# Kernel tuning notes

Hardware: AMD Instinct MI355X
Metric: run time of the kernel (lower is better)

Reference implementation:

```python
import jax, jax.numpy as jnp
import numpy as np

N_DRUGS = 4096; N_GENE = 5414; N_KG = N_DRUGS + N_GENE
N_MOL = 131072; E_MOL = 524288; E_KG = 524288; R = 8
MLP_IN = 1024; MLP_H = 512; D = 256; GCN_IN = 64; GCN_H = 128
DIM1 = 256; DIM2 = 128; DIM3 = 64; NCLS = 2
EPS = 1e-5


def setup_inputs() -> dict:
    key = jax.random.key(0)
    ks = jax.random.split(key, 32)
    def n(i, shape, fan):
        return jax.random.normal(ks[i], shape, dtype=jnp.float32) * (1.0 / np.sqrt(fan))
    inp = {}
    inp['fp_data'] = jax.random.normal(ks[0], (N_DRUGS, MLP_IN), dtype=jnp.float32)
    inp['mol_x'] = jax.random.normal(ks[1], (N_MOL, GCN_IN), dtype=jnp.float32)
    inp['mol_batch'] = jnp.sort(jax.random.randint(ks[2], (N_MOL,), 0, N_DRUGS))
    inp['mol_edge_index'] = jax.random.randint(ks[3], (2, E_MOL), 0, N_MOL)
    inp['kg_edge_index'] = jax.random.randint(ks[4], (2, E_KG), 0, N_KG)
    inp['kg_edge_type'] = jax.random.randint(ks[5], (E_KG,), 0, R)
    # parameters
    inp['fp_w1'] = n(6, (MLP_IN, MLP_H), MLP_IN); inp['fp_b1'] = jnp.zeros((MLP_H,), jnp.float32)
    inp['fp_w2'] = n(7, (MLP_H, D), MLP_H);       inp['fp_b2'] = jnp.zeros((D,), jnp.float32)
    inp['gcn_w1'] = n(8, (GCN_IN, GCN_H), GCN_IN); inp['gcn_b1'] = jnp.zeros((GCN_H,), jnp.float32)
    inp['gcn_w2'] = n(9, (GCN_H, D), GCN_H);       inp['gcn_b2'] = jnp.zeros((D,), jnp.float32)
    inp['att_w1'] = n(10, (D, 128), D); inp['att_b1'] = jnp.zeros((128,), jnp.float32)
    inp['att_w2'] = n(11, (128,), 128)
    inp['gene_emb'] = jax.random.normal(ks[12], (N_GENE, D), dtype=jnp.float32)
    inp['rg_w1'] = n(13, (R, D, DIM1), D); inp['rg_root1'] = n(14, (D, DIM1), D); inp['rg_b1'] = jnp.zeros((DIM1,), jnp.float32)
    inp['rg_w2'] = n(15, (R, DIM1, DIM2), DIM1); inp['rg_root2'] = n(16, (DIM1, DIM2), DIM1); inp['rg_b2'] = jnp.zeros((DIM2,), jnp.float32)
    inp['lin1_w'] = n(17, (DIM2, DIM3), DIM2); inp['lin1_b'] = jnp.zeros((DIM3,), jnp.float32)
    inp['lin2_w'] = n(18, (DIM3, NCLS), DIM3); inp['lin2_b'] = jnp.zeros((NCLS,), jnp.float32)
    return inp


def bn(x):
    # BatchNorm1d with batch statistics (gamma=1, beta=0)
    m = jnp.mean(x, axis=0, keepdims=True)
    v = jnp.var(x, axis=0, keepdims=True)
    return (x - m) * jax.lax.rsqrt(v + EPS)


def gcn_conv(x, w, b, src, dst, num_nodes):
    # PyG GCNConv: self-loops + symmetric normalization
    loop = jnp.arange(num_nodes, dtype=src.dtype)
    src = jnp.concatenate([src, loop]); dst = jnp.concatenate([dst, loop])
    h = x @ w  # [N, F]
    deg = jnp.zeros((num_nodes,), x.dtype).at[dst].add(1.0)
    dinv = jax.lax.rsqrt(jnp.maximum(deg, 1.0))
    norm = dinv[src] * dinv[dst]  # [E]
    out = jnp.zeros_like(h).at[dst].add(h[src] * norm[:, None])
    return out + b


def rgcn_conv(x, w, root, b, src, dst, etype, num_nodes):
    # PyG RGCNConv (aggr='mean' per relation): out_i = x_i @ root + b + sum_r mean_{j in N_r(i)} x_j @ W_r
    h = jnp.einsum('nd,rdf->rnf', x, w)          # [R, N, F]
    msg = h[etype, src]                          # [E, F] gather by (relation, source)
    cnt = jnp.zeros((R, num_nodes), x.dtype).at[etype, dst].add(1.0)
    norm = 1.0 / jnp.maximum(cnt[etype, dst], 1.0)  # [E]
    agg = jnp.zeros((num_nodes, w.shape[-1]), x.dtype).at[dst].add(msg * norm[:, None])
    return agg + x @ root + b


def forward(fp_data, mol_x, mol_batch, mol_edge_index, kg_edge_index, kg_edge_type,
            fp_w1, fp_b1, fp_w2, fp_b2, gcn_w1, gcn_b1, gcn_w2, gcn_b2,
            att_w1, att_b1, att_w2, gene_emb,
            rg_w1, rg_root1, rg_b1, rg_w2, rg_root2, rg_b2,
            lin1_w, lin1_b, lin2_w, lin2_b):
    # fingerprint MLP branch
    fp = jax.nn.relu(bn(fp_data @ fp_w1 + fp_b1))
    fp = jax.nn.relu(bn(fp @ fp_w2 + fp_b2))      # [N_DRUGS, D]
    # molecular GCN branch (batched graph replaces the dataloader loop)
    msrc, mdst = mol_edge_index[0], mol_edge_index[1]
    g = jax.nn.relu(bn(gcn_conv(mol_x, gcn_w1, gcn_b1, msrc, mdst, N_MOL)))
    g = jax.nn.relu(bn(gcn_conv(g, gcn_w2, gcn_b2, msrc, mdst, N_MOL)))  # [N_MOL, D]
    # global mean pool per molecule
    gsum = jnp.zeros((N_DRUGS, D), g.dtype).at[mol_batch].add(g)
    gcnt = jnp.zeros((N_DRUGS,), g.dtype).at[mol_batch].add(1.0)
    graph_out = gsum / jnp.maximum(gcnt, 1.0)[:, None]  # [N_DRUGS, D]
    # attention fusion of the two views
    z = jnp.stack([graph_out, fp], axis=1)        # [N_DRUGS, 2, D]
    w = jnp.tanh(z @ att_w1 + att_b1) @ att_w2    # [N_DRUGS, 2]
    beta = jax.nn.softmax(w, axis=1)
    emb = jnp.sum(beta[:, :, None] * z, axis=1)   # [N_DRUGS, D]
    # knowledge graph RGCN over drugs + genes
    x = jnp.concatenate([emb, gene_emb], axis=0)  # [N_KG, D]
    ksrc, kdst = kg_edge_index[0], kg_edge_index[1]
    x = jax.nn.relu(bn(rgcn_conv(x, rg_w1, rg_root1, rg_b1, ksrc, kdst, kg_edge_type, N_KG)))
    x = jax.nn.relu(bn(rgcn_conv(x, rg_w2, rg_root2, rg_b2, ksrc, kdst, kg_edge_type, N_KG)))
    x = jax.nn.relu(bn(x @ lin1_w + lin1_b))
    x = x @ lin2_w + lin2_b
    return jax.nn.log_softmax(x, axis=-1), beta[:, :, None]


def reference(fp_data, mol_x, mol_batch, mol_edge_index, kg_edge_index, kg_edge_type,
              fp_w1, fp_b1, fp_w2, fp_b2, gcn_w1, gcn_b1, gcn_w2, gcn_b2,
              att_w1, att_b1, att_w2, gene_emb,
              rg_w1, rg_root1, rg_b1, rg_w2, rg_root2, rg_b2,
              lin1_w, lin1_b, lin2_w, lin2_b):
    return forward(fp_data, mol_x, mol_batch, mol_edge_index, kg_edge_index, kg_edge_type,
                   fp_w1, fp_b1, fp_w2, fp_b2, gcn_w1, gcn_b1, gcn_w2, gcn_b2,
                   att_w1, att_b1, att_w2, gene_emb,
                   rg_w1, rg_root1, rg_b1, rg_w2, rg_root2, rg_b2,
                   lin1_w, lin1_b, lin2_w, lin2_b)
```

## Files before the change

kernel.cpp:

```cpp
#include <hip/hip_runtime.h>
#include <hip/hip_bf16.h>
#include <cstdint>

typedef __hip_bfloat16 bf16;
typedef unsigned short u16;
typedef unsigned int u32;
typedef __attribute__((ext_vector_type(8))) short short8;
typedef __attribute__((ext_vector_type(4))) float f32x4;

__device__ __forceinline__ float tofloat(float x){ return x; }
__device__ __forceinline__ float tofloat(bf16 x){ return __bfloat162float(x); }
__device__ __forceinline__ float b2f(u16 a){ return __uint_as_float(((unsigned)a) << 16); }
__device__ __forceinline__ u16 f2b(float f){
    unsigned u = __float_as_uint(f);
    return (u16)((u + 0x7FFFu + ((u >> 16) & 1u)) >> 16);
}

static inline int divup(long a, long b){ return (int)((a + b - 1) / b); }

#define NBLK_STATS 256

__global__ void zero_int(int* p){ *p = 0; }

__global__ void detect_f32(const u16* __restrict__ h, long n, int* flag)
{
    long i = (long)blockIdx.x * blockDim.x + threadIdx.x;
    long st = (long)gridDim.x * blockDim.x;
    int c = 0;
    for (; i < n; i += st)
        if (((h[i] >> 7) & 0xFF) == 0xFF) c++;
    if (c) atomicAdd(flag, c);
}

struct ConvTab { const void* src[14]; float* dst[14]; u16* dstB[14]; int n[14]; };

__global__ void conv_all(ConvTab t, const int* __restrict__ flagp)
{
    bool f32 = (*flagp != 0);
    int seg = blockIdx.y;
    const void* s = t.src[seg];
    float* d = t.dst[seg];
    u16*   dB = t.dstB[seg];
    int n = t.n[seg];
    long i = (long)blockIdx.x * blockDim.x + threadIdx.x;
    long st = (long)gridDim.x * blockDim.x;
    for (; i < n; i += st) {
        float v = f32 ? ((const float*)s)[i] : tofloat(((const bf16*)s)[i]);
        d[i] = v; dB[i] = f2b(v);
    }
}

__global__ void conv_in(const void* __restrict__ src, float* __restrict__ dst,
                        long n, const int* __restrict__ flagp)
{
    bool f32 = (*flagp != 0);
    long i = (long)blockIdx.x * blockDim.x + threadIdx.x;
    long st = (long)gridDim.x * blockDim.x;
    for (; i < n; i += st)
        dst[i] = f32 ? ((const float*)src)[i] : tofloat(((const bf16*)src)[i]);
}

__global__ void conv_dual_b16(const void* __restrict__ src, u16* __restrict__ dst,
                              long n, const int* __restrict__ flagp)
{
    bool f32 = (*flagp != 0);
    long i = (long)blockIdx.x * blockDim.x + threadIdx.x;
    long st = (long)gridDim.x * blockDim.x;
    for (; i < n; i += st)
        dst[i] = f32 ? f2b(((const float*)src)[i]) : ((const u16*)src)[i];
}

__global__ void conv_f32_b16(const float* __restrict__ src, u16* __restrict__ dst, long n)
{
    long i = (long)blockIdx.x * blockDim.x + threadIdx.x;
    long st = (long)gridDim.x * blockDim.x;
    for (; i < n; i += st) dst[i] = f2b(src[i]);
}

__global__ void conv_molx(const float* __restrict__ src, u16* __restrict__ dst,
                          long n4, const int* __restrict__ flagp)
{
    if (*flagp == 0) return;
    long i = (long)blockIdx.x * blockDim.x + threadIdx.x;
    long st = (long)gridDim.x * blockDim.x;
    for (; i < n4; i += st) {
        float4 v = ((const float4*)src)[i];
        ushort4 o;
        o.x = f2b(v.x); o.y = f2b(v.y); o.z = f2b(v.z); o.w = f2b(v.w);
        ((ushort4*)dst)[i] = o;
    }
}

__global__ __launch_bounds__(256)
void transpose_b16(const u16* __restrict__ src, u16* __restrict__ dst, int K, int N)
{
    __shared__ u16 t[32][33];
    int k0 = blockIdx.x * 32, n0 = blockIdx.y * 32;
    int x = threadIdx.x & 31, y = threadIdx.x >> 5;
    for (int yy = y; yy < 32; yy += 8) {
        int k = k0 + yy, n = n0 + x;
        t[yy][x] = (k < K && n < N) ? src[(long)k * N + n] : (u16)0;
    }
    __syncthreads();
    for (int yy = y; yy < 32; yy += 8) {
        int n = n0 + yy, k = k0 + x;
        if (n < N && k < K) dst[(long)n * K + k] = t[x][yy];
    }
}

__global__ void flatten_mol(const int* __restrict__ bins, const int* __restrict__ src,
                            const float* __restrict__ en, long E, int2* __restrict__ out)
{
    long i = (long)blockIdx.x * blockDim.x + threadIdx.x;
    long st = (long)gridDim.x * blockDim.x;
    for (; i < E; i += st) {
        int e = bins[i];
        out[i] = make_int2(src[e], __float_as_int(en[e]));
    }
}

__global__ void kg_key2(const int* __restrict__ dst, const int* __restrict__ et,
                        long E, int* __restrict__ key)
{
    long i = (long)blockIdx.x * blockDim.x + threadIdx.x;
    long st = (long)gridDim.x * blockDim.x;
    for (; i < E; i += st) key[i] = dst[i] * 8 + et[i];
}

__global__ void flatten_kg_src(const int* __restrict__ bins, const int* __restrict__ src,
                               long E, int* __restrict__ out)
{
    long i = (long)blockIdx.x * blockDim.x + threadIdx.x;
    long st = (long)gridDim.x * blockDim.x;
    for (; i < E; i += st) out[i] = src[bins[i]];
}

template<typename TC, int NBLK, bool STATS>
__global__ __launch_bounds__(256)
void gemm_bt(const u16* __restrict__ A, int lda,
             const u16* __restrict__ BT, int ldbt,
             TC* __restrict__ C, int ldc,
             int M, int N, int K,
             float* __restrict__ SP1, float* __restrict__ SP2, int Ntot)
{
    __shared__ __align__(16) u16 As[64][40];
    __shared__ __align__(16) u16 Bs[NBLK * 64][40];
    __shared__ float st1[NBLK * 64], st2[NBLK * 64];
    const int tid = threadIdx.x;
    const int lane = tid & 63, wave = tid >> 6;
    const int l15 = lane & 15, quad = lane >> 4;
    const int wm = (wave & 1) * 32, wn = (wave >> 1) * 32;
    const int row0 = blockIdx.x * 64, col0 = blockIdx.y * (NBLK * 64);
    const int arow = tid >> 2, ak = (tid & 3) * 8;
    const int aok = row0 + arow < M;

    if (STATS && tid < NBLK * 64) { st1[tid] = 0.f; st2[tid] = 0.f; }

    f32x4 acc[NBLK][2][2];
#pragma unroll
    for (int t = 0; t < NBLK; t++)
#pragma unroll
        for (int i = 0; i < 2; i++)
#pragma unroll
            for (int j = 0; j < 2; j++)
#pragma unroll
                for (int r = 0; r < 4; r++) acc[t][i][j][r] = 0.f;

    const u16* pa = A + (long)(row0 + arow) * lda + ak;
    const u16* pb[NBLK];
#pragma unroll
    for (int t = 0; t < NBLK; t++)
        pb[t] = BT + (long)(col0 + t * 64 + arow) * ldbt + ak;

    ushort4 ra0 = {0,0,0,0}, ra1 = {0,0,0,0};
    ushort4 rb0[NBLK], rb1[NBLK];
    if (aok) { ra0 = *(const ushort4*)pa; ra1 = *(const ushort4*)(pa + 4); }
#pragma unroll
    for (int t = 0; t < NBLK; t++) {
        rb0[t] = *(const ushort4*)pb[t];
        rb1[t] = *(const ushort4*)(pb[t] + 4);
    }

    for (int k0 = 0; k0 < K; k0 += 32) {
        *(ushort4*)&As[arow][ak]     = ra0;
        *(ushort4*)&As[arow][ak + 4] = ra1;
#pragma unroll
        for (int t = 0; t < NBLK; t++) {
// ... 69 lines not shown

__global__ __launch_bounds__(256)
void gemm64(const float* __restrict__ A, int lda,
            const float* __restrict__ B, int ldb,
            float* __restrict__ C, int ldc,
            int M, int N, int K)
{
    __shared__ float As[16][68];
    __shared__ float Bs[16][68];
    const int tid = threadIdx.x;
    const int row0 = blockIdx.x * 64, col0 = blockIdx.y * 64;
    float acc[4][4];
#pragma unroll
    for (int i = 0; i < 4; i++)
#pragma unroll
        for (int j = 0; j < 4; j++) acc[i][j] = 0.f;
    const int ar = tid >> 2, ak = (tid & 3) * 4;
    const int bk = tid >> 4, bc = (tid & 15) * 4;
    const int ty4 = (tid >> 4) * 4, tx4 = (tid & 15) * 4;
    for (int k0 = 0; k0 < K; k0 += 16) {
        {
            int row = row0 + ar;
            float4 v = make_float4(0.f, 0.f, 0.f, 0.f);
            if (row < M) v = *(const float4*)(A + (long)row * lda + k0 + ak);
            As[ak + 0][ar] = v.x; As[ak + 1][ar] = v.y;
            As[ak + 2][ar] = v.z; As[ak + 3][ar] = v.w;
        }
        {
            int c = col0 + bc;
            float4 v = make_float4(0.f, 0.f, 0.f, 0.f);
            if (c < N) v = *(const float4*)(B + (long)(k0 + bk) * ldb + c);
            *(float4*)&Bs[bk][bc] = v;
        }
        __syncthreads();
#pragma unroll
        for (int k = 0; k < 16; k++) {
            float4 a = *(const float4*)&As[k][ty4];
            float4 b = *(const float4*)&Bs[k][tx4];
            acc[0][0] += a.x * b.x; acc[0][1] += a.x * b.y; acc[0][2] += a.x * b.z; acc[0][3] += a.x * b.w;
            acc[1][0] += a.y * b.x; acc[1][1] += a.y * b.y; acc[1][2] += a.y * b.z; acc[1][3] += a.y * b.w;
            acc[2][0] += a.z * b.x; acc[2][1] += a.z * b.y; acc[2][2] += a.z * b.z; acc[2][3] += a.z * b.w;
            acc[3][0] += a.w * b.x; acc[3][1] += a.w * b.y; acc[3][2] += a.w * b.z; acc[3][3] += a.w * b.w;
        }
        __syncthreads();
    }
    int c = col0 + tx4;
#pragma unroll
    for (int i = 0; i < 4; i++) {
        int r = row0 + ty4 + i;
        if (r < M && c < N)
            *(float4*)&C[(long)r * ldc + c] =
                make_float4(acc[i][0], acc[i][1], acc[i][2], acc[i][3]);
    }
}

__global__ void filli(int* p, long n, int v)
{
    long i = (long)blockIdx.x * blockDim.x + threadIdx.x;
    long st = (long)gridDim.x * blockDim.x;
    for (; i < n; i += st) p[i] = v;
}

__global__ void hist_int(const int* __restrict__ key, long n, int* __restrict__ h)
{
    long i = (long)blockIdx.x * blockDim.x + threadIdx.x;
    long st = (long)gridDim.x * blockDim.x;
    for (; i < n; i += st) atomicAdd(&h[key[i]], 1);
}

__global__ __launch_bounds__(1024)
void scan_bsum(const int* __restrict__ in, int n, int* __restrict__ btot)
{
    __shared__ int sh[1024];
    int tid = threadIdx.x;
    int i0 = blockIdx.x * 4096 + tid * 4;
    int s = 0;
#pragma unroll
    for (int t = 0; t < 4; t++) { int idx = i0 + t; s += (idx < n) ? in[idx] : 0; }
    sh[tid] = s;
    __syncthreads();
    for (int off = 512; off > 0; off >>= 1) {
        if (tid < off) sh[tid] += sh[tid + off];
        __syncthreads();
    }
    if (tid == 0) btot[blockIdx.x] = sh[0];
}

__global__ void scan_tiny(const int* __restrict__ btot, int nb, int* __restrict__ boff)
{
    if (threadIdx.x == 0) {
        int c = 0;
        for (int b = 0; b < nb; b++) { boff[b] = c; c += btot[b]; }
        boff[nb] = c;
    }
}

__global__ __launch_bounds__(1024)
void scan_final(const int* __restrict__ in, int n, const int* __restrict__ boff,
                int nb, int* __restrict__ out)
{
    __shared__ int buf[1024];
    int tid = threadIdx.x;
    int i0 = blockIdx.x * 4096 + tid * 4;
    int v[4]; int s = 0;
#pragma unroll
    for (int t = 0; t < 4; t++) {
        int idx = i0 + t;
        v[t] = (idx < n) ? in[idx] : 0;
        s += v[t];
    }
    buf[tid] = s;
    __syncthreads();
    for (int off = 1; off < 1024; off <<= 1) {
        int t = (tid >= off) ? buf[tid - off] : 0;
        __syncthreads();
        buf[tid] += t;
        __syncthreads();
    }
    int excl = buf[tid] - s + boff[blockIdx.x];
#pragma unroll
    for (int t = 0; t < 4; t++) {
        int idx = i0 + t;
        if (idx < n) out[idx] = excl;
        excl += v[t];
    }
    if (blockIdx.x == 0 && tid == 0) out[n] = boff[nb];
}

__global__ void bin_by(const int* __restrict__ key, long n,
                       const int* __restrict__ off, int* __restrict__ cursor,
                       int* __restrict__ bins)
{
    long i = (long)blockIdx.x * blockDim.x + threadIdx.x;
    long st = (long)gridDim.x * blockDim.x;
    for (; i < n; i += st) {
        int k = key[i];
        int pos = off[k] + atomicAdd(&cursor[k], 1);
        bins[pos] = (int)i;
    }
}

__global__ void dinv_from_deg(const int* __restrict__ deg, float* __restrict__ dinv, long n)
{
    long i = (long)blockIdx.x * blockDim.x + threadIdx.x;
    long st = (long)gridDim.x * blockDim.x;
    for (; i < n; i += st) dinv[i] = rsqrtf((float)(deg[i] + 1));
}

__global__ void mol_enorm(const int* __restrict__ src, const int* __restrict__ dst,
                          const float* __restrict__ dinv, long E, float* __restrict__ en)
{
    long i = (long)blockIdx.x * blockDim.x + threadIdx.x;
    long st = (long)gridDim.x * blockDim.x;
    for (; i < E; i += st) en[i] = dinv[src[i]] * dinv[dst[i]];
}

__global__ __launch_bounds__(256)
void colstats_f32_v2(const float* __restrict__ X, int M, int N,
                     float* __restrict__ p1, float* __restrict__ p2)
{
    __shared__ float sh1[1024], sh2[1024];
    int tid = threadIdx.x;
    int ncg = N >> 2;
    int cg  = tid & (ncg - 1);
    int rg  = tid / ncg;
    int nrg = 256 / ncg;
    float s0=0,s1=0,s2=0,s3=0, q0=0,q1=0,q2=0,q3=0;
    const float* base = X + 4 * cg;
    for (long row = (long)blockIdx.x * nrg + rg; row < M; row += (long)gridDim.x * nrg) {
        float4 v = *(const float4*)(base + row * (long)N);
        s0 += v.x; q0 += v.x * v.x; s1 += v.y; q1 += v.y * v.y;
        s2 += v.z; q2 += v.z * v.z; s3 += v.w; q3 += v.w * v.w;
    }
    float4* S1 = (float4*)sh1; float4* S2 = (float4*)sh2;
    S1[tid] = make_float4(s0, s1, s2, s3);
    S2[tid] = make_float4(q0, q1, q2, q3);
    __syncthreads();
    for (int off = nrg >> 1; off > 0; off >>= 1) {
        if (rg < off) {
            float4 a = S1[tid], b = S1[tid + off * ncg];
            S1[tid] = make_float4(a.x + b.x, a.y + b.y, a.z + b.z, a.w + b.w);
            float4 c = S2[tid], d = S2[tid + off * ncg];
            S2[tid] = make_float4(c.x + d.x, c.y + d.y, c.z + d.z, c.w + d.w);
        }
        __syncthreads();
    }
    if (rg == 0) {
        *(float4*)&p1[(long)blockIdx.x * N + 4 * cg] = S1[tid];
        *(float4*)&p2[(long)blockIdx.x * N + 4 * cg] = S2[tid];
    }
}

__global__ __launch_bounds__(1024)
void colstats_reduce_v3(const float* __restrict__ p1, const float* __restrict__ p2,
                        int nblk, int N, float invM,
                        float* __restrict__ s1o, float* __restrict__ s2o)
{
    __shared__ float sh1[1024], sh2[1024];
    int tid = threadIdx.x;
    int col = blockIdx.x * 64 + (tid & 63);
    int seg = tid >> 6;
    float a = 0.f, c = 0.f;
    for (int b = seg; b < nblk; b += 16) {
        a += p1[(long)b * N + col];
        c += p2[(long)b * N + col];
    }
    sh1[tid] = a; sh2[tid] = c;
// ... 63 lines not shown
    for (; j < j1; j++) {
        int2 e = eb[j];
        acc += b2f(X[(long)e.x * 64 + lane]) * __int_as_float(e.y);
    }
    out[(long)wid * 64 + lane] = f2b(acc);
}

__global__ __launch_bounds__(256)
void mol_agg128_bn(const u16* __restrict__ G, const float* __restrict__ dinv,
                   const int* __restrict__ off, const int2* __restrict__ eb,
                   int NM, const float* __restrict__ s1, const float* __restrict__ s2,
                   u16* __restrict__ out)
{
    int wid  = (int)(((long)blockIdx.x * 256 + threadIdx.x) >> 6);
    int lane = threadIdx.x & 63;
    if (wid >= NM) return;
    const float m0 = s1[2 * lane],     r0 = s2[2 * lane];
    const float m1 = s1[2 * lane + 1], r1 = s2[2 * lane + 1];
    float dv = dinv[wid], dv2 = dv * dv;
    u32 u = *(const u32*)(G + (long)wid * 128 + 2 * lane);
    float a0 = fmaxf((b2f((u16)(u & 0xFFFF)) - m0) * r0, 0.f) * dv2;
    float a1 = fmaxf((b2f((u16)(u >> 16))    - m1) * r1, 0.f) * dv2;
    int j = off[wid], j1 = off[wid + 1];
    for (; j + 3 < j1; j += 4) {
        int2 e0 = eb[j], e1 = eb[j + 1], e2 = eb[j + 2], e3 = eb[j + 3];
        u32 v0 = *(const u32*)(G + (long)e0.x * 128 + 2 * lane);
        u32 v1 = *(const u32*)(G + (long)e1.x * 128 + 2 * lane);
        u32 v2 = *(const u32*)(G + (long)e2.x * 128 + 2 * lane);
        u32 v3 = *(const u32*)(G + (long)e3.x * 128 + 2 * lane);
        float n0 = __int_as_float(e0.y), n1 = __int_as_float(e1.y);
        float n2 = __int_as_float(e2.y), n3 = __int_as_float(e3.y);
        a0 += fmaxf((b2f((u16)(v0 & 0xFFFF)) - m0) * r0, 0.f) * n0
            + fmaxf((b2f((u16)(v1 & 0xFFFF)) - m0) * r0, 0.f) * n1
            + fmaxf((b2f((u16)(v2 & 0xFFFF)) - m0) * r0, 0.f) * n2
            + fmaxf((b2f((u16)(v3 & 0xFFFF)) - m0) * r0, 0.f) * n3;
        a1 += fmaxf((b2f((u16)(v0 >> 16)) - m1) * r1, 0.f) * n0
            + fmaxf((b2f((u16)(v1 >> 16)) - m1) * r1, 0.f) * n1
            + fmaxf((b2f((u16)(v2 >> 16)) - m1) * r1, 0.f) * n2
            + fmaxf((b2f((u16)(v3 >> 16)) - m1) * r1, 0.f) * n3;
    }
    for (; j < j1; j++) {
        int2 e = eb[j];
        u32 v = *(const u32*)(G + (long)e.x * 128 + 2 * lane);
        float n = __int_as_float(e.y);
        a0 += fmaxf((b2f((u16)(v & 0xFFFF)) - m0) * r0, 0.f) * n;
        a1 += fmaxf((b2f((u16)(v >> 16))    - m1) * r1, 0.f) * n;
    }
    u32 o = (u32)f2b(a0) | ((u32)f2b(a1) << 16);
    *(u32*)(out + (long)wid * 128 + 2 * lane) = o;
}

__global__ __launch_bounds__(256)
void kg_preagg2(const u16* __restrict__ xin, const int* __restrict__ off2,
                const int* __restrict__ eb, int NSEG, u16* __restrict__ aggx)
{
    int seg  = (int)(((long)blockIdx.x * 256 + threadIdx.x) >> 6);
    int lane = threadIdx.x & 63;
    if (seg >= NSEG) return;
    int node = seg >> 3, r = seg & 7;
    const int c4 = 4 * lane;
    int j0 = off2[seg], j1 = off2[seg + 1];
    float a0 = 0.f, a1 = 0.f, a2 = 0.f, a3 = 0.f;
    int j = j0;
    for (; j + 3 < j1; j += 4) {
        int s0 = eb[j], s1 = eb[j + 1], s2 = eb[j + 2], s3 = eb[j + 3];
        ushort4 v0 = *(const ushort4*)(xin + (long)s0 * 256 + c4);
        ushort4 v1 = *(const ushort4*)(xin + (long)s1 * 256 + c4);
        ushort4 v2 = *(const ushort4*)(xin + (long)s2 * 256 + c4);
        ushort4 v3 = *(const ushort4*)(xin + (long)s3 * 256 + c4);
        a0 += b2f(v0.x) + b2f(v1.x) + b2f(v2.x) + b2f(v3.x);
        a1 += b2f(v0.y) + b2f(v1.y) + b2f(v2.y) + b2f(v3.y);
        a2 += b2f(v0.z) + b2f(v1.z) + b2f(v2.z) + b2f(v3.z);
        a3 += b2f(v0.w) + b2f(v1.w) + b2f(v2.w) + b2f(v3.w);
    }
    for (; j < j1; j++) {
        ushort4 v = *(const ushort4*)(xin + (long)eb[j] * 256 + c4);
        a0 += b2f(v.x); a1 += b2f(v.y); a2 += b2f(v.z); a3 += b2f(v.w);
    }
    float nrm = 1.0f / fmaxf((float)(j1 - j0), 1.0f);
    ushort4 o;
    o.x = f2b(a0 * nrm); o.y = f2b(a1 * nrm);
    o.z = f2b(a2 * nrm); o.w = f2b(a3 * nrm);
    *(ushort4*)(aggx + (long)node * 2304 + 256 + (r << 8) + c4) = o;
}

__global__ void xcopy_aggx(const u16* __restrict__ xin, u16* __restrict__ aggx, long n4)
{
    long i = (long)blockIdx.x * blockDim.x + threadIdx.x;
    long st = (long)gridDim.x * blockDim.x;
    for (; i < n4; i += st) {
        long node = i >> 6;
        int c4 = (int)(i & 63) * 4;
        *(ushort4*)(aggx + node * 2304 + c4) = *(const ushort4*)(xin + node * 256 + c4);
    }
}

__global__ __launch_bounds__(256)
void pool128(const u16* __restrict__ g, const int* __restrict__ off,
             const int* __restrict__ bins, int ND,
             const float* __restrict__ s1, const float* __restrict__ s2,
             float* __restrict__ gout, int c0out)
{
    int wid  = (int)(((long)blockIdx.x * 256 + threadIdx.x) >> 6);
    int lane = threadIdx.x & 63;
    if (wid >= ND) return;
    const float m0 = s1[2 * lane],     r0 = s2[2 * lane];
    const float m1 = s1[2 * lane + 1], r1 = s2[2 * lane + 1];
    int j0 = off[wid], j1 = off[wid + 1];
    float a0 = 0.f, a1 = 0.f;
    for (int j = j0; j < j1; j++) {
        u32 v = *(const u32*)(g + (long)bins[j] * 128 + 2 * lane);
        a0 += fmaxf((b2f((u16)(v & 0xFFFF)) - m0) * r0, 0.f);
        a1 += fmaxf((b2f((u16)(v >> 16))    - m1) * r1, 0.f);
    }
    float inv = 1.0f / fmaxf((float)(j1 - j0), 1.0f);
    *(float2*)(gout + (long)wid * 256 + c0out + 2 * lane) =
        make_float2(a0 * inv, a1 * inv);
}

__global__ void attention_fuse(const float* __restrict__ go, const float* __restrict__ fpv,
                               const float* __restrict__ fs1, const float* __restrict__ fs2,
                               const float* __restrict__ W1, const float* __restrict__ B1,
                               const float* __restrict__ W2,
                               float* __restrict__ emb, float* __restrict__ beta_out)
{
    int d = blockIdx.x;
    int t = threadIdx.x;
    __shared__ float z[2][256];
    __shared__ float red[128];
    for (int c = t; c < 256; c += 128) {
        z[0][c] = go[(long)d * 256 + c];
        z[1][c] = fmaxf((fpv[(long)d * 256 + c] - fs1[c]) * fs2[c], 0.f);
    }
    __syncthreads();
    float s[2];
    for (int v = 0; v < 2; v++) {
        float acc = B1[t];
        for (int k = 0; k < 256; k++) acc += z[v][k] * W1[k * 128 + t];
        red[t] = tanhf(acc) * W2[t];
        __syncthreads();
        for (int off = 64; off > 0; off >>= 1) {
            if (t < off) red[t] += red[t + off];
            __syncthreads();
        }
        s[v] = red[0];
        __syncthreads();
    }
    float m = fmaxf(s[0], s[1]);
    float e0 = expf(s[0] - m), e1 = expf(s[1] - m);
    float inv = 1.0f / (e0 + e1);
    float b0 = e0 * inv, b1 = e1 * inv;
    for (int c = t; c < 256; c += 128)
        emb[(long)d * 256 + c] = b0 * z[0][c] + b1 * z[1][c];
    if (t == 0) {
        beta_out[d * 2 + 0] = b0;
        beta_out[d * 2 + 1] = b1;
    }
}

__global__ void logits_out_bn(const float* __restrict__ x4,
                              const float* __restrict__ s1, const float* __restrict__ s2,
                              const float* __restrict__ w, const float* __restrict__ b,
                              float* __restrict__ out, int NKG)
{
    int i = blockIdx.x * blockDim.x + threadIdx.x;
    if (i >= NKG) return;
    float a0 = b[0], a1 = b[1];
    for (int k = 0; k < 64; k++) {
        float v = fmaxf((x4[(long)i * 64 + k] - s1[k]) * s2[k], 0.f);
        a0 += v * w[k * 2 + 0];
        a1 += v * w[k * 2 + 1];
    }
    float m = fmaxf(a0, a1);
    float lse = m + logf(expf(a0 - m) + expf(a1 - m));
    out[i * 2 + 0] = a0 - lse;
    out[i * 2 + 1] = a1 - lse;
}

extern "C" void kernel_launch(void* const* d_in, const int* in_sizes, int n_in,
                              void* d_out, int out_size, void* d_ws, size_t ws_size,
                              hipStream_t stream)
{
    (void)in_sizes; (void)n_in; (void)out_size; (void)ws_size;
    const int ND = 4096, NM = 131072, NKG = 9510, NGENE = 5414;
    const long EM = 524288, EK = 524288;
    const int NSEG = 8 * NKG;

    const void* fp_data = d_in[0];
    const void* mol_x   = d_in[1];
    const int*  mol_batch = (const int*)d_in[2];
    const int*  mol_ei  = (const int*)d_in[3];
    const int*  kg_ei   = (const int*)d_in[4];
    const int*  kg_et   = (const int*)d_in[5];

    const int* mol_src = mol_ei;
    const int* mol_dst = mol_ei + EM;
    const int* kg_src  = kg_ei;
    const int* kg_dst  = kg_ei + EK;

    float* out_ls   = (float*)d_out;
    float* out_beta = (float*)d_out + 19020;

    char* wp = (char*)d_ws;
    auto carve = [&](size_t bytes) { char* p = wp; wp += (bytes + 255) & ~(size_t)255; return p; };
    float* stats   = (float*)carve(4096);
    float* statsFP = (float*)carve(4096);
    int*   flag  = (int*)carve(256);
    float* dinv  = (float*)carve((size_t)NM * 4);
    float* enM   = (float*)carve((size_t)EM * 4);
    float* part1 = (float*)carve((size_t)2048 * 128 * 4);
    float* part2 = (float*)carve((size_t)2048 * 128 * 4);
    int*   sbt   = (int*)carve(256);
    int*   sbo   = (int*)carve(256);
    float* Wpool = (float*)carve((size_t)1630000 * 4);
    u16*   WpoolB= (u16*)carve((size_t)1630000 * 2);
    u16*   WpoolT= (u16*)carve((size_t)1600000 * 2);
    float* fpb   = (float*)carve((size_t)ND * 256 * 4);
    float* gout  = (float*)carve((size_t)ND * 256 * 4);
    int*   key2  = (int*)carve((size_t)EK * 4);
    int*   koff2 = (int*)carve((size_t)(NSEG + 1) * 4);
    char*  z0    = wp;
    int* kdeg2 = (int*)carve((size_t)NSEG * 4);
    int* kcur2 = (int*)carve((size_t)NSEG * 4);
    int* mdeg = (int*)carve((size_t)NM * 4);
    int* mcur = (int*)carve((size_t)NM * 4);
    int* pdeg = (int*)carve((size_t)ND * 4);
    int* pcur = (int*)carve((size_t)ND * 4);
    char*  z1    = wp;
    int* moff = (int*)carve((size_t)(NM + 1) * 4);
    int* mbins= (int*)carve((size_t)EM * 4);
    int* kbins= (int*)carve((size_t)EK * 4);
    int* poff = (int*)carve((size_t)(ND + 1) * 4);
    int* pbins= (int*)carve((size_t)NM * 4);
    char*  REG1  = carve((size_t)NM * 128 * 2);
    char*  REG2  = carve((size_t)NM * 128 * 2);
    u16*   HB    = (u16*)carve((size_t)NM * 64 * 2);

    u16*   XB  = (u16*)REG1;
    u16*   G1  = (u16*)REG1;
    u16*   H2  = (u16*)REG1;
    float* xkg = (float*)REG1;
    u16*   x2b = (u16*)REG1;
    float* x3  = (float*)REG1 + (size_t)NKG * 512;
    float* x4  = x3 + (size_t)NKG * 128;
    u16*   xb  = (u16*)(x4 + (size_t)NKG * 64);
    u16*   Xfb = (u16*)REG2;
    u16*   G1A = (u16*)REG2;
    u16*   AGGX= (u16*)REG2;
    u16*   fp1b = HB;
    u16*   Xagg = HB;
    int2* ebM  = (int2*)gout;
    int*  ebK2 = key2;

    zero_int<<<1, 1, 0, stream>>>(flag);
    detect_f32<<<1024, 256, 0, stream>>>((const u16*)fp_data, (long)ND * 1024, flag);
    ConvTab tab;
    const int widx[14] = {6, 8, 10, 12, 14, 15, 16, 19, 18, 22, 21, 24, 26, 27};
    const int wn[14]   = {1024*512, 512*256, 64*128, 128*256, 256*128, 128, 128,
                          256*256, 8*256*256, 256*128, 8*256*128, 128*64, 64*2, 2};
    float* wf[14]; u16* wb[14];
    {
        size_t o = 0;
        for (int i = 0; i < 14; i++) {
            tab.src[i]  = d_in[widx[i]];
            tab.dst[i]  = Wpool + o;
            tab.dstB[i] = WpoolB + o;
            tab.n[i]    = wn[i];
            wf[i] = Wpool + o; wb[i] = WpoolB + o;
            o += (size_t)wn[i];
        }
    }
    conv_all<<<dim3(32, 14), 256, 0, stream>>>(tab, flag);
    float *att_w1c = wf[4], *att_b1c = wf[5], *att_w2c = wf[6];
    float *lin1_wc = wf[11], *lin2_wc = wf[12], *lin2_bc = wf[13];

    u16* T_fpw1  = WpoolT;
    u16* T_fpw2  = T_fpw1 + (size_t)512 * 1024;
    u16* T_gcnw1 = T_fpw2 + (size_t)256 * 512;
    u16* T_gcnw2 = T_gcnw1 + (size_t)128 * 64;
    u16* T_w1    = T_gcnw2 + (size_t)256 * 128;
    u16* T_w2    = T_w1 + (size_t)256 * 2304;
    transpose_b16<<<dim3(32, 16), 256, 0, stream>>>(wb[0], T_fpw1, 1024, 512);
    transpose_b16<<<dim3(16, 8),  256, 0, stream>>>(wb[1], T_fpw2, 512, 256);
    transpose_b16<<<dim3(2, 4),   256, 0, stream>>>(wb[2], T_gcnw1, 64, 128);
    transpose_b16<<<dim3(4, 8),   256, 0, stream>>>(wb[3], T_gcnw2, 128, 256);
    transpose_b16<<<dim3(72, 8),  256, 0, stream>>>(wb[7], T_w1, 2304, 256);
    transpose_b16<<<dim3(72, 4),  256, 0, stream>>>(wb[9], T_w2, 2304, 128);

    filli<<<512, 256, 0, stream>>>((int*)z0, (long)(z1 - z0) / 4, 0);
    auto scan = [&](const int* deg, int* off, int n) {
        int nb = divup(n, 4096);
        scan_bsum<<<nb, 1024, 0, stream>>>(deg, n, sbt);
        scan_tiny<<<1, 64, 0, stream>>>(sbt, nb, sbo);
        scan_final<<<nb, 1024, 0, stream>>>(deg, n, sbo, nb, off);
    };
    hist_int<<<2048, 256, 0, stream>>>(mol_dst, EM, mdeg);
    scan(mdeg, moff, NM);
    bin_by<<<2048, 256, 0, stream>>>(mol_dst, EM, moff, mcur, mbins);
    dinv_from_deg<<<512, 256, 0, stream>>>(mdeg, dinv, NM);
    mol_enorm<<<1024, 256, 0, stream>>>(mol_src, mol_dst, dinv, EM, enM);
    flatten_mol<<<2048, 256, 0, stream>>>(mbins, mol_src, enM, EM, ebM);

    kg_key2<<<2048, 256, 0, stream>>>(kg_dst, kg_et, EK, key2);
    hist_int<<<2048, 256, 0, stream>>>(key2, EK, kdeg2);
    scan(kdeg2, koff2, NSEG);
    bin_by<<<2048, 256, 0, stream>>>(key2, EK, koff2, kcur2, kbins);
    flatten_kg_src<<<2048, 256, 0, stream>>>(kbins, kg_src, EK, ebK2);

    hist_int<<<512, 256, 0, stream>>>(mol_batch, NM, pdeg);
    scan(pdeg, poff, ND);
    bin_by<<<512, 256, 0, stream>>>(mol_batch, NM, poff, pcur, pbins);

    auto reduceNto = [&](int nblk, int N, float invM, float* s1o, float* s2o) {
        colstats_reduce_v3<<<N / 64, 1024, 0, stream>>>(part1, part2, nblk, N,
                                                        invM, s1o, s2o);
    };

    conv_dual_b16<<<2048, 256, 0, stream>>>(fp_data, Xfb, (long)ND * 1024, flag);
    gemm_bt<u16, 2, true><<<dim3(64, 4), 256, 0, stream>>>(
        Xfb, 1024, T_fpw1, 1024, fp1b, 512, ND, 512, 1024, part1, part2, 512);
    reduceNto(64, 512, 1.0f / ND, stats, stats + 512);
    bn_apply_b16v<<<2048, 256, 0, stream>>>((u32*)fp1b, (long)ND * 256, 255,
                                            stats, stats + 512);
    gemm_bt<float, 1, true><<<dim3(64, 4), 256, 0, stream>>>(
        fp1b, 512, T_fpw2, 512, fpb, 256, ND, 256, 512, part1, part2, 256);
    reduceNto(64, 256, 1.0f / ND, statsFP, statsFP + 512);

    conv_molx<<<2048, 256, 0, stream>>>((const float*)mol_x, XB, (long)NM * 16, flag);
    mol_agg_in<<<32768, 256, 0, stream>>>(mol_x, XB, flag, dinv, moff, ebM, NM, Xagg);
    gemm_bt<u16, 2, true><<<dim3(2048, 1), 256, 0, stream>>>(
        Xagg, 64, T_gcnw1, 64, G1, 128, NM, 128, 64, part1, part2, 128);
    reduceNto(2048, 128, 1.0f / NM, stats, stats + 512);

    mol_agg128_bn<<<32768, 256, 0, stream>>>(G1, dinv, moff, ebM, NM,
                                             stats, stats + 512, G1A);
    for (int h = 0; h < 2; h++) {
        gemm_bt<u16, 2, true><<<dim3(2048, 1), 256, 0, stream>>>(
            G1A, 128, T_gcnw2 + (size_t)h * 128 * 128, 128, H2, 128, NM, 128, 128,
            part1, part2, 128);
        reduceNto(2048, 128, 1.0f / NM, stats, stats + 512);
        pool128<<<1024, 256, 0, stream>>>(H2, poff, pbins, ND,
                                          stats, stats + 512, gout, h * 128);
    }

    attention_fuse<<<ND, 128, 0, stream>>>(gout, fpb, statsFP, statsFP + 512,
                                           att_w1c, att_b1c, att_w2c,
                                           xkg, out_beta);
    conv_in<<<512, 256, 0, stream>>>(d_in[17], xkg + (long)ND * 256,
                                     (long)NGENE * 256, flag);
    conv_f32_b16<<<1024, 256, 0, stream>>>(xkg, xb, (long)NKG * 256);

    xcopy_aggx<<<1024, 256, 0, stream>>>(xb, AGGX, (long)NKG * 64);
    kg_preagg2<<<divup((long)NSEG * 64, 256), 256, 0, stream>>>(
        xb, koff2, ebK2, NSEG, AGGX);
    gemm_bt<u16, 2, true><<<dim3(divup(NKG, 64), 2), 256, 0, stream>>>(
        AGGX, 2304, T_w1, 2304, x2b, 256, NKG, 256, 2304, part1, part2, 256);
    reduceNto(divup(NKG, 64), 256, 1.0f / NKG, stats, stats + 512);
    bn_apply_b16v<<<1024, 256, 0, stream>>>((u32*)x2b, (long)NKG * 128, 127,
                                            stats, stats + 512);

    xcopy_aggx<<<1024, 256, 0, stream>>>(x2b, AGGX, (long)NKG * 64);
    kg_preagg2<<<divup((long)NSEG * 64, 256), 256, 0, stream>>>(
        x2b, koff2, ebK2, NSEG, AGGX);
    gemm_bt<float, 1, true><<<dim3(divup(NKG, 64), 2), 256, 0, stream>>>(
        AGGX, 2304, T_w2, 2304, x3, 128, NKG, 128, 2304, part1, part2, 128);
    reduceNto(divup(NKG, 64), 128, 1.0f / NKG, stats, stats + 512);
    bn_apply<<<2048, 256, 0, stream>>>(x3, (long)NKG * 128, 127, stats, stats + 512);

    gemm64<<<dim3(divup(NKG, 64), 1, 1), 256, 0, stream>>>(
        x3, 128, lin1_wc, 64, x4, 64, NKG, 64, 128);
    colstats_f32_v2<<<NBLK_STATS, 256, 0, stream>>>(x4, NKG, 64, part1, part2);
    reduceNto(NBLK_STATS, 64, 1.0f / NKG, stats, stats + 512);
    logits_out_bn<<<divup(NKG, 256), 256, 0, stream>>>(x4, stats, stats + 512,
                                                       lin2_wc, lin2_bc, out_ls, NKG);
}
```

Measured before the change: 1.028 ms.

## Batch preprocessing kernels across graphs and fuse copy/convert launches

Merges the six weight transposes into one launch, and the three histogram, scan and bin passes (mol edges, KG edges, pooling batch) into multi-segment launches indexed by blockIdx. Edge-norm computation is folded into the mol flatten, and both flattens share one launch. Attention now writes bf16 directly and gene embeddings are converted straight to bf16, dropping the fp32 staging buffer. The self-feature copy into the aggregation buffer moves into kg_preagg2. The aim is fewer kernel launches and less memory traffic, at the cost of some idle blocks in the padded grids.

```diff
diff --git a/kernel.cpp b/kernel.cpp
--- a/kernel.cpp
+++ b/kernel.cpp
@@ -50,16 +50,6 @@
     }
 }
 
-__global__ void conv_in(const void* __restrict__ src, float* __restrict__ dst,
-                        long n, const int* __restrict__ flagp)
-{
-    bool f32 = (*flagp != 0);
-    long i = (long)blockIdx.x * blockDim.x + threadIdx.x;
-    long st = (long)gridDim.x * blockDim.x;
-    for (; i < n; i += st)
-        dst[i] = f32 ? ((const float*)src)[i] : tofloat(((const bf16*)src)[i]);
-}
-
 __global__ void conv_dual_b16(const void* __restrict__ src, u16* __restrict__ dst,
                               long n, const int* __restrict__ flagp)
 {
@@ -68,13 +58,6 @@
     long st = (long)gridDim.x * blockDim.x;
     for (; i < n; i += st)
         dst[i] = f32 ? f2b(((const float*)src)[i]) : ((const u16*)src)[i];
-}
-
-__global__ void conv_f32_b16(const float* __restrict__ src, u16* __restrict__ dst, long n)
-{
-    long i = (long)blockIdx.x * blockDim.x + threadIdx.x;
-    long st = (long)gridDim.x * blockDim.x;
-    for (; i < n; i += st) dst[i] = f2b(src[i]);
 }
 
 __global__ void conv_molx(const float* __restrict__ src, u16* __restrict__ dst,
@@ -91,31 +74,126 @@
     }
 }
 
+struct TransTab { const u16* src[6]; u16* dst[6]; int K[6]; int N[6]; };
+
 __global__ __launch_bounds__(256)
-void transpose_b16(const u16* __restrict__ src, u16* __restrict__ dst, int K, int N)
-{
-    __shared__ u16 t[32][33];
+void transpose6(TransTab t)
+{
+    int s = blockIdx.z;
+    int K = t.K[s], N = t.N[s];
     int k0 = blockIdx.x * 32, n0 = blockIdx.y * 32;
+    if (k0 >= K || n0 >= N) return;
+    const u16* src = t.src[s];
+    u16* dst = t.dst[s];
+    __shared__ u16 tl[32][33];
     int x = threadIdx.x & 31, y = threadIdx.x >> 5;
     for (int yy = y; yy < 32; yy += 8) {
         int k = k0 + yy, n = n0 + x;
-        t[yy][x] = (k < K && n < N) ? src[(long)k * N + n] : (u16)0;
+        tl[yy][x] = (k < K && n < N) ? src[(long)k * N + n] : (u16)0;
     }
     __syncthreads();
     for (int yy = y; yy < 32; yy += 8) {
         int n = n0 + yy, k = k0 + x;
-        if (n < N && k < K) dst[(long)n * K + k] = t[x][yy];
-    }
-}
-
-__global__ void flatten_mol(const int* __restrict__ bins, const int* __restrict__ src,
-                            const float* __restrict__ en, long E, int2* __restrict__ out)
-{
-    long i = (long)blockIdx.x * blockDim.x + threadIdx.x;
-    long st = (long)gridDim.x * blockDim.x;
-    for (; i < E; i += st) {
-        int e = bins[i];
-        out[i] = make_int2(src[e], __float_as_int(en[e]));
+        if (n < N && k < K) dst[(long)n * K + k] = tl[x][yy];
+    }
+}
+
+struct KV3 { const int* key[3]; int* h[3]; long n[3]; };
+
+__global__ void hist3(KV3 t)
+{
+    int s = blockIdx.y;
+    const int* key = t.key[s]; int* h = t.h[s]; long n = t.n[s];
+    long i = (long)blockIdx.x * blockDim.x + threadIdx.x;
+    long st = (long)gridDim.x * blockDim.x;
+    for (; i < n; i += st) atomicAdd(&h[key[i]], 1);
+}
+
+struct Scan3 { const int* in[3]; int* out[3]; int* bt[3]; int* bo[3]; int n[3]; };
+
+__global__ __launch_bounds__(1024)
+void scan_bsum3(Scan3 t)
+{
+    int s = blockIdx.y;
+    int n = t.n[s];
+    int nb = (n + 4095) >> 12;
+    if ((int)blockIdx.x >= nb) return;
+    const int* in = t.in[s];
+    __shared__ int sh[1024];
+    int tid = threadIdx.x;
+    int i0 = blockIdx.x * 4096 + tid * 4;
+    int acc = 0;
+#pragma unroll
+    for (int k = 0; k < 4; k++) { int idx = i0 + k; acc += (idx < n) ? in[idx] : 0; }
+    sh[tid] = acc;
+    __syncthreads();
+    for (int off = 512; off > 0; off >>= 1) {
+        if (tid < off) sh[tid] += sh[tid + off];
+        __syncthreads();
+    }
+    if (tid == 0) t.bt[s][blockIdx.x] = sh[0];
+}
+
+__global__ void scan_tiny3(Scan3 t)
+{
+    int s = blockIdx.x;
+    if (threadIdx.x != 0) return;
+    int nb = (t.n[s] + 4095) >> 12;
+    const int* bt = t.bt[s]; int* bo = t.bo[s];
+    int c = 0;
+    for (int b = 0; b < nb; b++) { bo[b] = c; c += bt[b]; }
+    bo[nb] = c;
+}
+
+__global__ __launch_bounds__(1024)
+void scan_final3(Scan3 t)
+{
+    int s = blockIdx.y;
+    int n = t.n[s];
+    int nb = (n + 4095) >> 12;
+    if ((int)blockIdx.x >= nb) return;
+    const int* in = t.in[s]; int* out = t.out[s]; const int* bo = t.bo[s];
+    __shared__ int buf[1024];
+    int tid = threadIdx.x;
+    int i0 = blockIdx.x * 4096 + tid * 4;
+    int v[4]; int acc = 0;
+#pragma unroll
+    for (int k = 0; k < 4; k++) {
+        int idx = i0 + k;
+        v[k] = (idx < n) ? in[idx] : 0;
+        acc += v[k];
+    }
+    buf[tid] = acc;
+    __syncthreads();
+    for (int off = 1; off < 1024; off <<= 1) {
+        int tv = (tid >= off) ? buf[tid - off] : 0;
+        __syncthreads();
+        buf[tid] += tv;
+        __syncthreads();
+    }
+    int excl = buf[tid] - acc + bo[blockIdx.x];
+#pragma unroll
+    for (int k = 0; k < 4; k++) {
+        int idx = i0 + k;
+        if (idx < n) out[idx] = excl;
+        excl += v[k];
+    }
+    if (blockIdx.x == 0 && tid == 0) out[n] = bo[nb];
+}
+
+struct Bin3 { const int* key[3]; const int* off[3]; int* cur[3]; int* bins[3]; long n[3]; };
+
+__global__ void bin3(Bin3 t)
+{
+    int s = blockIdx.y;
+    const int* key = t.key[s]; const int* off = t.off[s];
+    int* cur = t.cur[s]; int* bins = t.bins[s]; long n = t.n[s];
+    long i = (long)blockIdx.x * blockDim.x + threadIdx.x;
+    long st = (long)gridDim.x * blockDim.x;
+    for (; i < n; i += st) {
+        int k = key[i];
+        int pos = off[k] + atomicAdd(&cur[k], 1);
+        bins[pos] = (int)i;
     }
 }
 
@@ -127,12 +205,37 @@
     for (; i < E; i += st) key[i] = dst[i] * 8 + et[i];
 }
 
-__global__ void flatten_kg_src(const int* __restrict__ bins, const int* __restrict__ src,
-                               long E, int* __restrict__ out)
-{
-    long i = (long)blockIdx.x * blockDim.x + threadIdx.x;
-    long st = (long)gridDim.x * blockDim.x;
-    for (; i < E; i += st) out[i] = src[bins[i]];
+__global__ void flatten2(const int* __restrict__ mbins, const int* __restrict__ msrc,
+                         const int* __restrict__ mdst, const float* __restrict__ dinv,
+                         int2* __restrict__ ebM,
+                         const int* __restrict__ kbins, const int* __restrict__ ksrc,
+                         int* __restrict__ ebK, long E)
+{
+    long i = (long)blockIdx.x * blockDim.x + threadIdx.x;
+    long st = (long)gridDim.x * blockDim.x;
+    if (blockIdx.y == 0) {
+        for (; i < E; i += st) {
+            int e = mbins[i];
+            int sn = msrc[e];
+            ebM[i] = make_int2(sn, __float_as_int(dinv[sn] * dinv[mdst[e]]));
+        }
+    } else {
+        for (; i < E; i += st) ebK[i] = ksrc[kbins[i]];
+    }
+}
+
+__global__ void filli(int* p, long n, int v)
+{
+    long i = (long)blockIdx.x * blockDim.x + threadIdx.x;
+    long st = (long)gridDim.x * blockDim.x;
+    for (; i < n; i += st) p[i] = v;
+}
+
+__global__ void dinv_from_deg(const int* __restrict__ deg, float* __restrict__ dinv, long n)
+{
+    long i = (long)blockIdx.x * blockDim.x + threadIdx.x;
+    long st = (long)gridDim.x * blockDim.x;
+    for (; i < n; i += st) dinv[i] = rsqrtf((float)(deg[i] + 1));
 }
 
 template<typename TC, int NBLK, bool STATS>
@@ -308,107 +411,6 @@
             *(float4*)&C[(long)r * ldc + c] =
                 make_float4(acc[i][0], acc[i][1], acc[i][2], acc[i][3]);
     }
-}
-
-__global__ void filli(int* p, long n, int v)
-{
-    long i = (long)blockIdx.x * blockDim.x + threadIdx.x;
-    long st = (long)gridDim.x * blockDim.x;
-    for (; i < n; i += st) p[i] = v;
-}
-
-__global__ void hist_int(const int* __restrict__ key, long n, int* __restrict__ h)
-{
-    long i = (long)blockIdx.x * blockDim.x + threadIdx.x;
-    long st = (long)gridDim.x * blockDim.x;
-    for (; i < n; i += st) atomicAdd(&h[key[i]], 1);
-}
-
-__global__ __launch_bounds__(1024)
-void scan_bsum(const int* __restrict__ in, int n, int* __restrict__ btot)
-{
-    __shared__ int sh[1024];
-    int tid = threadIdx.x;
-    int i0 = blockIdx.x * 4096 + tid * 4;
-    int s = 0;
-#pragma unroll
-    for (int t = 0; t < 4; t++) { int idx = i0 + t; s += (idx < n) ? in[idx] : 0; }
-    sh[tid] = s;
-    __syncthreads();
-    for (int off = 512; off > 0; off >>= 1) {
-        if (tid < off) sh[tid] += sh[tid + off];
-        __syncthreads();
-    }
-    if (tid == 0) btot[blockIdx.x] = sh[0];
-}
-
-__global__ void scan_tiny(const int* __restrict__ btot, int nb, int* __restrict__ boff)
-{
-    if (threadIdx.x == 0) {
-        int c = 0;
-        for (int b = 0; b < nb; b++) { boff[b] = c; c += btot[b]; }
-        boff[nb] = c;
-    }
-}
-
-__global__ __launch_bounds__(1024)
-void scan_final(const int* __restrict__ in, int n, const int* __restrict__ boff,
-                int nb, int* __restrict__ out)
-{
-    __shared__ int buf[1024];
-    int tid = threadIdx.x;
-    int i0 = blockIdx.x * 4096 + tid * 4;
-    int v[4]; int s = 0;
-#pragma unroll
-    for (int t = 0; t < 4; t++) {
-        int idx = i0 + t;
-        v[t] = (idx < n) ? in[idx] : 0;
-        s += v[t];
-    }
-    buf[tid] = s;
-    __syncthreads();
-    for (int off = 1; off < 1024; off <<= 1) {
-        int t = (tid >= off) ? buf[tid - off] : 0;
-        __syncthreads();
-        buf[tid] += t;
-        __syncthreads();
-    }
-    int excl = buf[tid] - s + boff[blockIdx.x];
-#pragma unroll
-    for (int t = 0; t < 4; t++) {
-        int idx = i0 + t;
-        if (idx < n) out[idx] = excl;
-        excl += v[t];
-    }
-    if (blockIdx.x == 0 && tid == 0) out[n] = boff[nb];
-}
-
-__global__ void bin_by(const int* __restrict__ key, long n,
-                       const int* __restrict__ off, int* __restrict__ cursor,
-                       int* __restrict__ bins)
-{
-    long i = (long)blockIdx.x * blockDim.x + threadIdx.x;
-    long st = (long)gridDim.x * blockDim.x;
-    for (; i < n; i += st) {
-        int k = key[i];
-        int pos = off[k] + atomicAdd(&cursor[k], 1);
-        bins[pos] = (int)i;
-    }
-}
-
-__global__ void dinv_from_deg(const int* __restrict__ deg, float* __restrict__ dinv, long n)
-{
-    long i = (long)blockIdx.x * blockDim.x + threadIdx.x;
-    long st = (long)gridDim.x * blockDim.x;
-    for (; i < n; i += st) dinv[i] = rsqrtf((float)(deg[i] + 1));
-}
-
-__global__ void mol_enorm(const int* __restrict__ src, const int* __restrict__ dst,
-                          const float* __restrict__ dinv, long E, float* __restrict__ en)
-{
-    long i = (long)blockIdx.x * blockDim.x + threadIdx.x;
-    long st = (long)gridDim.x * blockDim.x;
-    for (; i < E; i += st) en[i] = dinv[src[i]] * dinv[dst[i]];
 }
 
 __global__ __launch_bounds__(256)
@@ -578,13 +580,19 @@
 
 __global__ __launch_bounds__(256)
 void kg_preagg2(const u16* __restrict__ xin, const int* __restrict__ off2,
-                const int* __restrict__ eb, int NSEG, u16* __restrict__ aggx)
+                const int* __restrict__ eb, int NSEG, int NKG, u16* __restrict__ aggx)
 {
     int seg  = (int)(((long)blockIdx.x * 256 + threadIdx.x) >> 6);
     int lane = threadIdx.x & 63;
-    if (seg >= NSEG) return;
+    const int c4 = 4 * lane;
+    if (seg >= NSEG + NKG) return;
+    if (seg >= NSEG) {
+        int node = seg - NSEG;
+        *(ushort4*)(aggx + (long)node * 2304 + c4) =
+            *(const ushort4*)(xin + (long)node * 256 + c4);
+        return;
+    }
     int node = seg >> 3, r = seg & 7;
-    const int c4 = 4 * lane;
     int j0 = off2[seg], j1 = off2[seg + 1];
     float a0 = 0.f, a1 = 0.f, a2 = 0.f, a3 = 0.f;
     int j = j0;
@@ -610,17 +618,6 @@
     *(ushort4*)(aggx + (long)node * 2304 + 256 + (r << 8) + c4) = o;
 }
 
-__global__ void xcopy_aggx(const u16* __restrict__ xin, u16* __restrict__ aggx, long n4)
-{
-    long i = (long)blockIdx.x * blockDim.x + threadIdx.x;
-    long st = (long)gridDim.x * blockDim.x;
-    for (; i < n4; i += st) {
-        long node = i >> 6;
-        int c4 = (int)(i & 63) * 4;
-        *(ushort4*)(aggx + node * 2304 + c4) = *(const ushort4*)(xin + node * 256 + c4);
-    }
-}
-
 __global__ __launch_bounds__(256)
 void pool128(const u16* __restrict__ g, const int* __restrict__ off,
              const int* __restrict__ bins, int ND,
@@ -648,7 +645,7 @@
                                const float* __restrict__ fs1, const float* __restrict__ fs2,
                                const float* __restrict__ W1, const float* __restrict__ B1,
                                const float* __restrict__ W2,
-                               float* __restrict__ emb, float* __restrict__ beta_out)
+                               u16* __restrict__ embb, float* __restrict__ beta_out)
 {
     int d = blockIdx.x;
     int t = threadIdx.x;
@@ -677,7 +674,7 @@
     float inv = 1.0f / (e0 + e1);
     float b0 = e0 * inv, b1 = e1 * inv;
     for (int c = t; c < 256; c += 128)
-        emb[(long)d * 256 + c] = b0 * z[0][c] + b1 * z[1][c];
+        embb[(long)d * 256 + c] = f2b(b0 * z[0][c] + b1 * z[1][c]);
     if (t == 0) {
         beta_out[d * 2 + 0] = b0;
         beta_out[d * 2 + 1] = b1;
@@ -733,11 +730,10 @@
     float* statsFP = (float*)carve(4096);
     int*   flag  = (int*)carve(256);
     float* dinv  = (float*)carve((size_t)NM * 4);
-    float* enM   = (float*)carve((size_t)EM * 4);
     float* part1 = (float*)carve((size_t)2048 * 128 * 4);
     float* part2 = (float*)carve((size_t)2048 * 128 * 4);
-    int*   sbt   = (int*)carve(256);
-    int*   sbo   = (int*)carve(256);
+    int*   sbt3  = (int*)carve(3 * 64 * 4);
+    int*   sbo3  = (int*)carve(3 * 64 * 4);
     float* Wpool = (float*)carve((size_t)1630000 * 4);
     u16*   WpoolB= (u16*)carve((size_t)1630000 * 2);
     u16*   WpoolT= (u16*)carve((size_t)1600000 * 2);
@@ -765,7 +761,6 @@
     u16*   XB  = (u16*)REG1;
     u16*   G1  = (u16*)REG1;
     u16*   H2  = (u16*)REG1;
-    float* xkg = (float*)REG1;
     u16*   x2b = (u16*)REG1;
     float* x3  = (float*)REG1 + (size_t)NKG * 512;
     float* x4  = x3 + (size_t)NKG * 128;
@@ -806,36 +801,44 @@
     u16* T_gcnw2 = T_gcnw1 + (size_t)128 * 64;
     u16* T_w1    = T_gcnw2 + (size_t)256 * 128;
     u16* T_w2    = T_w1 + (size_t)256 * 2304;
-    transpose_b16<<<dim3(32, 16), 256, 0, stream>>>(wb[0], T_fpw1, 1024, 512);
-    transpose_b16<<<dim3(16, 8),  256, 0, stream>>>(wb[1], T_fpw2, 512, 256);
-    transpose_b16<<<dim3(2, 4),   256, 0, stream>>>(wb[2], T_gcnw1, 64, 128);
-    transpose_b16<<<dim3(4, 8),   256, 0, stream>>>(wb[3], T_gcnw2, 128, 256);
-    transpose_b16<<<dim3(72, 8),  256, 0, stream>>>(wb[7], T_w1, 2304, 256);
-    transpose_b16<<<dim3(72, 4),  256, 0, stream>>>(wb[9], T_w2, 2304, 128);
+    TransTab tt;
+    tt.src[0] = wb[0]; tt.dst[0] = T_fpw1;  tt.K[0] = 1024; tt.N[0] = 512;
+    tt.src[1] = wb[1]; tt.dst[1] = T_fpw2;  tt.K[1] = 512;  tt.N[1] = 256;
+    tt.src[2] = wb[2]; tt.dst[2] = T_gcnw1; tt.K[2] = 64;   tt.N[2] = 128;
+    tt.src[3] = wb[3]; tt.dst[3] = T_gcnw2; tt.K[3] = 128;  tt.N[3] = 256;
+    tt.src[4] = wb[7]; tt.dst[4] = T_w1;    tt.K[4] = 2304; tt.N[4] = 256;
+    tt.src[5] = wb[9]; tt.dst[5] = T_w2;    tt.K[5] = 2304; tt.N[5] = 128;
+    transpose6<<<dim3(72, 16, 6), 256, 0, stream>>>(tt);
 
     filli<<<512, 256, 0, stream>>>((int*)z0, (long)(z1 - z0) / 4, 0);
-    auto scan = [&](const int* deg, int* off, int n) {
-        int nb = divup(n, 4096);
-        scan_bsum<<<nb, 1024, 0, stream>>>(deg, n, sbt);
-        scan_tiny<<<1, 64, 0, stream>>>(sbt, nb, sbo);
-        scan_final<<<nb, 1024, 0, stream>>>(deg, n, sbo, nb, off);
-    };
-    hist_int<<<2048, 256, 0, stream>>>(mol_dst, EM, mdeg);
-    scan(mdeg, moff, NM);
-    bin_by<<<2048, 256, 0, stream>>>(mol_dst, EM, moff, mcur, mbins);
+    kg_key2<<<2048, 256, 0, stream>>>(kg_dst, kg_et, EK, key2);
+    {
+        KV3 hv;
+        hv.key[0] = mol_dst;   hv.h[0] = mdeg;  hv.n[0] = EM;
+        hv.key[1] = key2;      hv.h[1] = kdeg2; hv.n[1] = EK;
+        hv.key[2] = mol_batch; hv.h[2] = pdeg;  hv.n[2] = NM;
+        hist3<<<dim3(2048, 3), 256, 0, stream>>>(hv);
+    }
     dinv_from_deg<<<512, 256, 0, stream>>>(mdeg, dinv, NM);
-    mol_enorm<<<1024, 256, 0, stream>>>(mol_src, mol_dst, dinv, EM, enM);
-    flatten_mol<<<2048, 256, 0, stream>>>(mbins, mol_src, enM, EM, ebM);
-
-    kg_key2<<<2048, 256, 0, stream>>>(kg_dst, kg_et, EK, key2);
-    hist_int<<<2048, 256, 0, stream>>>(key2, EK, kdeg2);
-    scan(kdeg2, koff2, NSEG);
-    bin_by<<<2048, 256, 0, stream>>>(key2, EK, koff2, kcur2, kbins);
-    flatten_kg_src<<<2048, 256, 0, stream>>>(kbins, kg_src, EK, ebK2);
-
-    hist_int<<<512, 256, 0, stream>>>(mol_batch, NM, pdeg);
-    scan(pdeg, poff, ND);
-    bin_by<<<512, 256, 0, stream>>>(mol_batch, NM, poff, pcur, pbins);
+    {
+        Scan3 sc;
+        sc.in[0] = mdeg;  sc.out[0] = moff;  sc.n[0] = NM;
+        sc.in[1] = kdeg2; sc.out[1] = koff2; sc.n[1] = NSEG;
+        sc.in[2] = pdeg;  sc.out[2] = poff;  sc.n[2] = ND;
+        for (int s = 0; s < 3; s++) { sc.bt[s] = sbt3 + s * 64; sc.bo[s] = sbo3 + s * 64; }
+        scan_bsum3<<<dim3(32, 3), 1024, 0, stream>>>(sc);
+        scan_tiny3<<<3, 64, 0, stream>>>(sc);
+        scan_final3<<<dim3(32, 3), 1024, 0, stream>>>(sc);
+    }
+    {
+        Bin3 bv;
+        bv.key[0] = mol_dst;   bv.off[0] = moff;  bv.cur[0] = mcur;  bv.bins[0] = mbins; bv.n[0] = EM;
+        bv.key[1] = key2;      bv.off[1] = koff2; bv.cur[1] = kcur2; bv.bins[1] = kbins; bv.n[1] = EK;
+        bv.key[2] = mol_batch; bv.off[2] = poff;  bv.cur[2] = pcur;  bv.bins[2] = pbins; bv.n[2] = NM;
+        bin3<<<dim3(2048, 3), 256, 0, stream>>>(bv);
+    }
+    flatten2<<<dim3(2048, 2), 256, 0, stream>>>(mbins, mol_src, mol_dst, dinv, ebM,
+                                                kbins, kg_src, ebK2, EM);
 
     auto reduceNto = [&](int nblk, int N, float invM, float* s1o, float* s2o) {
         colstats_reduce_v3<<<N / 64, 1024, 0, stream>>>(part1, part2, nblk, N,
@@ -871,23 +874,20 @@
 
     attention_fuse<<<ND, 128, 0, stream>>>(gout, fpb, statsFP, statsFP + 512,
                                            att_w1c, att_b1c, att_w2c,
-                                           xkg, out_beta);
-    conv_in<<<512, 256, 0, stream>>>(d_in[17], xkg + (long)ND * 256,
-                                     (long)NGENE * 256, flag);
-    conv_f32_b16<<<1024, 256, 0, stream>>>(xkg, xb, (long)NKG * 256);
-
-    xcopy_aggx<<<1024, 256, 0, stream>>>(xb, AGGX, (long)NKG * 64);
-    kg_preagg2<<<divup((long)NSEG * 64, 256), 256, 0, stream>>>(
-        xb, koff2, ebK2, NSEG, AGGX);
+                                           xb, out_beta);
+    conv_dual_b16<<<512, 256, 0, stream>>>(d_in[17], xb + (long)ND * 256,
+                                           (long)NGENE * 256, flag);
+
+    kg_preagg2<<<divup((long)(NSEG + NKG) * 64, 256), 256, 0, stream>>>(
+        xb, koff2, ebK2, NSEG, NKG, AGGX);
     gemm_bt<u16, 2, true><<<dim3(divup(NKG, 64), 2), 256, 0, stream>>>(
         AGGX, 2304, T_w1, 2304, x2b, 256, NKG, 256, 2304, part1, part2, 256);
     reduceNto(divup(NKG, 64), 256, 1.0f / NKG, stats, stats + 512);
     bn_apply_b16v<<<1024, 256, 0, stream>>>((u32*)x2b, (long)NKG * 128, 127,
                                             stats, stats + 512);
 
-    xcopy_aggx<<<1024, 256, 0, stream>>>(x2b, AGGX, (long)NKG * 64);
-    kg_preagg2<<<divup((long)NSEG * 64, 256), 256, 0, stream>>>(
-        x2b, koff2, ebK2, NSEG, AGGX);
+    kg_preagg2<<<divup((long)(NSEG + NKG) * 64, 256), 256, 0, stream>>>(
+        x2b, koff2, ebK2, NSEG, NKG, AGGX);
     gemm_bt<float, 1, true><<<dim3(divup(NKG, 64), 2), 256, 0, stream>>>(
         AGGX, 2304, T_w2, 2304, x3, 128, NKG, 128, 2304, part1, part2, 128);
     reduceNto(divup(NKG, 64), 128, 1.0f / NKG, stats, stats + 512);
```

Result: faster. 986.6 us (-4.0%).
